# Performance work log

Hardware: AMD Instinct MI355X
Metric: run time of the kernel (lower is better)

The kernel has to match this reference:

```python
import jax, jax.numpy as jnp
import numpy as np

NF, NH1, NH21, NH22, NCLS = 6, 128, 128, 128, 3
OBS_X, OBS_Y, OBS_Z, R = 10.0, 10.0, 9.0, 7.0
BATCH = 131072


def setup_inputs() -> dict:
    key = jax.random.key(0)
    ks = jax.random.split(key, 16)
    def lin(kw, kb, fan_in, fan_out):
        bound = 1.0 / np.sqrt(fan_in)
        w = jax.random.uniform(kw, (fan_out, fan_in), jnp.float32, -bound, bound)
        b = jax.random.uniform(kb, (fan_out,), jnp.float32, -bound, bound)
        return w, b
    fc1_w, fc1_b = lin(ks[0], ks[1], NF, NH1)
    fc21_w, fc21_b = lin(ks[2], ks[3], NH1, NH21)
    fc22_w, fc22_b = lin(ks[4], ks[5], NH1, NH22)
    fcm1_w, fcm1_b = lin(ks[6], ks[7], NH21, NH21)
    fcm2_w, fcm2_b = lin(ks[8], ks[9], NH22, NH22)
    fc31_w, fc31_b = lin(ks[10], ks[11], NH21, NCLS)
    fc32_w, fc32_b = lin(ks[12], ks[13], NH22, 2)
    x = jax.random.normal(ks[14], (BATCH, NF), jnp.float32)
    mean = jnp.array([10.0, 0.0, 10.0, 0.0, 9.0, 0.0], jnp.float32)
    std = jnp.array([5.0, 2.0, 5.0, 2.0, 5.0, 2.0], jnp.float32)
    return {"x": x, "mean": mean, "std": std,
            "fc1_w": fc1_w, "fc1_b": fc1_b,
            "fc21_w": fc21_w, "fc21_b": fc21_b,
            "fc22_w": fc22_w, "fc22_b": fc22_b,
            "fcm1_w": fcm1_w, "fcm1_b": fcm1_b,
            "fcm2_w": fcm2_w, "fcm2_b": fcm2_b,
            "fc31_w": fc31_w, "fc31_b": fc31_b,
            "fc32_w": fc32_w, "fc32_b": fc32_b,
            "sgn": 1}


def _forward(x, mean, std, fc1_w, fc1_b, fc21_w, fc21_b, fc22_w, fc22_b,
             fcm1_w, fcm1_b, fcm2_w, fcm2_b, fc31_w, fc31_b, fc32_w, fc32_b):
    x0 = x * std + mean                                   # de-normalized state [B,6]
    h = jnp.tanh(x @ fc1_w.T + fc1_b)                     # [B,NH1]
    x21 = jnp.tanh(h @ fc21_w.T + fc21_b)
    x22 = jnp.tanh(h @ fc22_w.T + fc22_b)
    x21 = jnp.tanh(x21 @ fcm1_w.T + fcm1_b)
    x22 = jnp.tanh(x22 @ fcm2_w.T + fcm2_b)
    x31 = x21 @ fc31_w.T + fc31_b                         # QP linear term p, [B,3]
    x32 = 4.0 * jax.nn.sigmoid(x22 @ fc32_w.T + fc32_b)   # HOCBF penalties, [B,2]

    # higher-order CBF terms
    px, vx, py, vy, pz, vz = (x0[:, i] for i in range(6))
    dx, dy, dz = px - OBS_X, py - OBS_Y, pz - OBS_Z
    barrier = dx**4 + dy**4 + dz**4 - R**4
    barrier_dot = 4.0 * (dx**3 * vx + dy**3 * vy + dz**3 * vz)
    Lf2b = 12.0 * (dx**2 * vx**2 + dy**2 * vy**2 + dz**2 * vz**2)
    G = -4.0 * jnp.stack([dx**3, dy**3, dz**3], axis=-1)  # [B,3], single constraint G u <= h
    hvec = Lf2b + (x32[:, 0] + x32[:, 1]) * barrier_dot + x32[:, 0] * x32[:, 1] * barrier  # [B]

    # QP: min 0.5 u^T u + x31^T u  s.t.  G u <= h  (Q = I, one constraint)
    # Closed-form KKT: u = -x31 - lam*G, lam = max(0, (G @ (-x31) - h) / (G @ G))
    u_unc = -x31
    Gu = jnp.sum(G * u_unc, axis=-1)                      # [B]
    GG = jnp.sum(G * G, axis=-1)                          # [B]
    lam = jnp.maximum(Gu - hvec, 0.0) / GG
    u = u_unc - lam[:, None] * G                          # [B,3]
    return u


def reference(x, mean, std, fc1_w, fc1_b, fc21_w, fc21_b, fc22_w, fc22_b,
              fcm1_w, fcm1_b, fcm2_w, fcm2_b, fc31_w, fc31_b, fc32_w, fc32_b, sgn):
    return _forward(x, mean, std, fc1_w, fc1_b, fc21_w, fc21_b, fc22_w, fc22_b,
                    fcm1_w, fcm1_b, fcm2_w, fcm2_b, fc31_w, fc31_b, fc32_w, fc32_b)
```

## Files before the change

kernel.cpp:

```cpp
#include <hip/hip_runtime.h>

typedef _Float16 half8 __attribute__((ext_vector_type(8)));
typedef _Float16 half4_t __attribute__((ext_vector_type(4)));
typedef float float4_t __attribute__((ext_vector_type(4)));
typedef float float2_t __attribute__((ext_vector_type(2)));

#define SB 32
#define NT 256
#define RS (SB * 8)

#define OFF_W1   0
#define OFF_W21  4096
#define OFF_W22  20480
#define OFF_WM1  36864
#define OFF_WM2  53248
#define OFF_W4A  69632
#define OFF_BIAS 73728
#define WS_HELEMS 73728

__device__ __forceinline__ float fast_tanh(float x) {
  float e = __builtin_amdgcn_exp2f(x * 2.8853900817779268f);
  return fmaf(-2.f, __builtin_amdgcn_rcpf(1.f + e), 1.f);
}
__device__ __forceinline__ float sigmoid4(float z) {
  float e = __builtin_amdgcn_exp2f(-z * 1.4426950408889634f);
  return 4.f * __builtin_amdgcn_rcpf(1.f + e);
}

__global__ void prepack(const float* __restrict__ w1, const float* __restrict__ w21,
                        const float* __restrict__ w22, const float* __restrict__ wm1,
                        const float* __restrict__ wm2, const float* __restrict__ w31,
                        const float* __restrict__ w32, const float* __restrict__ b1,
                        const float* __restrict__ b21, const float* __restrict__ b22,
                        const float* __restrict__ bm1, const float* __restrict__ bm2,
                        _Float16* __restrict__ ws) {
  const int stride = gridDim.x * blockDim.x;
  for (int i = blockIdx.x * blockDim.x + threadIdx.x; i < WS_HELEMS; i += stride) {
    float v;
    if (i < OFF_W21) {
      int t = i;
      int j = t & 7, c = t >> 3, l16 = c & 15, t1 = c >> 4;
      int k8 = t1 & 3, mt = t1 >> 2;
      int row = mt * 16 + l16, k = k8 * 8 + j;
      v = (k < 6) ? w1[row * 6 + k] : 0.f;
    } else if (i < OFF_W4A) {
      int t = i - OFF_W21;
      int m = t >> 14; t &= 16383;
      const float* src = (m == 0) ? w21 : (m == 1) ? w22 : (m == 2) ? wm1 : wm2;
      int j = t & 7, c = t >> 3, l16 = c & 15, t1 = c >> 4;
      int k8 = t1 & 15, mt = t1 >> 4;
      v = src[(mt * 16 + l16) * 128 + k8 * 8 + j];
    } else {
      int t = i - OFF_W4A;
      int j = t & 7, r = t >> 3, l16 = r & 15, q = r >> 4;
      int cc = q & 15, chain = q >> 4;
      int k = cc * 8 + j, m = l16;
      if (chain == 0) v = (m < 3) ? w31[m * 128 + k] : 0.f;
      else            v = (m < 2) ? w32[m * 128 + k] : 0.f;
    }
    ws[i] = (_Float16)v;
  }
  float* bws = (float*)(ws + OFF_BIAS);
  for (int i = blockIdx.x * blockDim.x + threadIdx.x; i < 640; i += stride) {
    int layer = i >> 7, idx = i & 127;
    const float* src = (layer == 0) ? b1 : (layer == 1) ? b21
                     : (layer == 2) ? b22 : (layer == 3) ? bm1 : bm2;
    bws[i] = src[idx];
  }
}

__device__ __forceinline__ void gemm128(const _Float16* __restrict__ Wg,
                                        const float* __restrict__ biasG,
                                        const _Float16* __restrict__ inB,
                                        _Float16* __restrict__ outB,
                                        int quad, int l16, int mt0, int mt1) {
  const float4_t bv0 = *(const float4_t*)(biasG + mt0 * 16 + quad * 4);
  const float4_t bv1 = *(const float4_t*)(biasG + mt1 * 16 + quad * 4);
  half8 a0[4], a1[4];
#pragma unroll
  for (int kk = 0; kk < 4; ++kk) {
    a0[kk] = *(const half8*)(Wg + ((mt0 * 16 + kk * 4 + quad) * 16 + l16) * 8);
    a1[kk] = *(const half8*)(Wg + ((mt1 * 16 + kk * 4 + quad) * 16 + l16) * 8);
  }
  float4_t acc0[2], acc1[2];
#pragma unroll
  for (int nt = 0; nt < 2; ++nt) {
    acc0[nt] = (float4_t){0.f, 0.f, 0.f, 0.f};
    acc1[nt] = (float4_t){0.f, 0.f, 0.f, 0.f};
  }
#pragma unroll
  for (int kk = 0; kk < 4; ++kk) {
#pragma unroll
    for (int nt = 0; nt < 2; ++nt) {
      half8 b = *(const half8*)(inB + (kk * 4 + quad) * RS + (nt * 16 + l16) * 8);
      acc0[nt] = __builtin_amdgcn_mfma_f32_16x16x32_f16(a0[kk], b, acc0[nt], 0, 0, 0);
      acc1[nt] = __builtin_amdgcn_mfma_f32_16x16x32_f16(a1[kk], b, acc1[nt], 0, 0, 0);
    }
  }
  const int ob0 = mt0 * 16 + quad * 4;
  const int ob1 = mt1 * 16 + quad * 4;
#pragma unroll
  for (int nt = 0; nt < 2; ++nt) {
    const int s = nt * 16 + l16;
    half4_t h0, h1;
#pragma unroll
    for (int r = 0; r < 4; ++r) {
      h0[r] = (_Float16)fast_tanh(acc0[nt][r] + bv0[r]);
      h1[r] = (_Float16)fast_tanh(acc1[nt][r] + bv1[r]);
    }
    *(half4_t*)(outB + (ob0 >> 3) * RS + s * 8 + (ob0 & 7)) = h0;
    *(half4_t*)(outB + (ob1 >> 3) * RS + s * 8 + (ob1 & 7)) = h1;
  }
}

__global__ __launch_bounds__(NT, 6) void bnet_main(
    const float* __restrict__ x, const float* __restrict__ meang,
    const float* __restrict__ stdg, const float* __restrict__ b31,
    const float* __restrict__ b32, const _Float16* __restrict__ ws,
    float* __restrict__ out) {
  __shared__ __align__(16) _Float16 bufH[SB * 128];
  __shared__ __align__(16) _Float16 bufA[SB * 128];
  __shared__ __align__(16) _Float16 bufB[SB * 128];

  const int tid = threadIdx.x;
  const int wv = tid >> 6;
  const int lane = tid & 63;
  const int quad = lane >> 4;
  const int l16 = lane & 15;
  const int mt0 = wv * 2, mt1 = mt0 + 1;
  const int s0 = blockIdx.x * SB;
  const float* biasF = (const float*)(ws + OFF_BIAS);

  {
    half8 bx[2];
#pragma unroll
    for (int nt = 0; nt < 2; ++nt) {
      half8 v;
#pragma unroll
      for (int j = 0; j < 8; ++j) v[j] = (_Float16)0.f;
      if (quad == 0) {
        const float* xp = x + (size_t)(s0 + nt * 16 + l16) * 6;
        float2_t e0 = *(const float2_t*)(xp);
        float2_t e1 = *(const float2_t*)(xp + 2);
        float2_t e2 = *(const float2_t*)(xp + 4);
        v[0] = (_Float16)e0[0]; v[1] = (_Float16)e0[1];
        v[2] = (_Float16)e1[0]; v[3] = (_Float16)e1[1];
        v[4] = (_Float16)e2[0]; v[5] = (_Float16)e2[1];
      }
      bx[nt] = v;
    }
    const float4_t bv0 = *(const float4_t*)(biasF + mt0 * 16 + quad * 4);
    const float4_t bv1 = *(const float4_t*)(biasF + mt1 * 16 + quad * 4);
    half8 a0 = *(const half8*)(ws + OFF_W1 + ((mt0 * 4 + quad) * 16 + l16) * 8);
    half8 a1 = *(const half8*)(ws + OFF_W1 + ((mt1 * 4 + quad) * 16 + l16) * 8);
    float4_t acc0[2], acc1[2];
#pragma unroll
    for (int nt = 0; nt < 2; ++nt) {
      acc0[nt] = (float4_t){0.f, 0.f, 0.f, 0.f};
      acc1[nt] = (float4_t){0.f, 0.f, 0.f, 0.f};
      acc0[nt] = __builtin_amdgcn_mfma_f32_16x16x32_f16(a0, bx[nt], acc0[nt], 0, 0, 0);
      acc1[nt] = __builtin_amdgcn_mfma_f32_16x16x32_f16(a1, bx[nt], acc1[nt], 0, 0, 0);
    }
    const int ob0 = mt0 * 16 + quad * 4;
    const int ob1 = mt1 * 16 + quad * 4;
#pragma unroll
    for (int nt = 0; nt < 2; ++nt) {
      const int s = nt * 16 + l16;
      half4_t h0, h1;
#pragma unroll
      for (int r = 0; r < 4; ++r) {
        h0[r] = (_Float16)fast_tanh(acc0[nt][r] + bv0[r]);
        h1[r] = (_Float16)fast_tanh(acc1[nt][r] + bv1[r]);
      }
      *(half4_t*)(bufH + (ob0 >> 3) * RS + s * 8 + (ob0 & 7)) = h0;
      *(half4_t*)(bufH + (ob1 >> 3) * RS + s * 8 + (ob1 & 7)) = h1;
    }
  }
  __syncthreads();

  gemm128(ws + OFF_W21, biasF + 128, bufH, bufA, quad, l16, mt0, mt1);
  gemm128(ws + OFF_W22, biasF + 256, bufH, bufB, quad, l16, mt0, mt1);
  __syncthreads();
  gemm128(ws + OFF_WM1, biasF + 384, bufA, bufH, quad, l16, mt0, mt1);
  __syncthreads();
  gemm128(ws + OFF_WM2, biasF + 512, bufB, bufA, quad, l16, mt0, mt1);
  __syncthreads();

  if (wv == 0) {
    half8 a4[2][4];
#pragma unroll
    for (int c = 0; c < 2; ++c)
#pragma unroll
      for (int kk = 0; kk < 4; ++kk)
        a4[c][kk] = *(const half8*)(ws + OFF_W4A +
                                    ((c * 16 + kk * 4 + quad) * 16 + l16) * 8);
    float4_t acc[2][2];
#pragma unroll
    for (int c = 0; c < 2; ++c)
#pragma unroll
      for (int nt = 0; nt < 2; ++nt) acc[c][nt] = (float4_t){0.f, 0.f, 0.f, 0.f};
#pragma unroll
    for (int kk = 0; kk < 4; ++kk)
#pragma unroll
      for (int nt = 0; nt < 2; ++nt) {
        half8 b1f = *(const half8*)(bufH + (kk * 4 + quad) * RS + (nt * 16 + l16) * 8);
        half8 b2f = *(const half8*)(bufA + (kk * 4 + quad) * RS + (nt * 16 + l16) * 8);
        acc[0][nt] = __builtin_amdgcn_mfma_f32_16x16x32_f16(a4[0][kk], b1f, acc[0][nt], 0, 0, 0);
        acc[1][nt] = __builtin_amdgcn_mfma_f32_16x16x32_f16(a4[1][kk], b2f, acc[1][nt], 0, 0, 0);
      }
    if (quad == 0) {
      const float m0 = meang[0], m1 = meang[1], m2 = meang[2];
      const float m3 = meang[3], m4 = meang[4], m5 = meang[5];
      const float sd0 = stdg[0], sd1 = stdg[1], sd2 = stdg[2];
      const float sd3 = stdg[3], sd4 = stdg[4], sd5 = stdg[5];
      const float c31_0 = b31[0], c31_1 = b31[1], c31_2 = b31[2];
      const float c32_0 = b32[0], c32_1 = b32[1];
#pragma unroll
      for (int nt = 0; nt < 2; ++nt) {
        const int s = nt * 16 + l16;
        float u0 = -(acc[0][nt][0] + c31_0);
        float u1 = -(acc[0][nt][1] + c31_1);
        float u2 = -(acc[0][nt][2] + c31_2);
        float p0 = sigmoid4(acc[1][nt][0] + c32_0);
        float p1 = sigmoid4(acc[1][nt][1] + c32_1);
        const float* xp = x + (size_t)(s0 + s) * 6;
        float2_t e0 = *(const float2_t*)(xp);
        float2_t e1 = *(const float2_t*)(xp + 2);
        float2_t e2 = *(const float2_t*)(xp + 4);
        float px = e0[0] * sd0 + m0, vx = e0[1] * sd1 + m1;
        float py = e1[0] * sd2 + m2, vy = e1[1] * sd3 + m3;
        float pz = e2[0] * sd4 + m4, vz = e2[1] * sd5 + m5;
        float dx = px - 10.f, dy = py - 10.f, dz = pz - 9.f;
        float dx2 = dx * dx, dy2 = dy * dy, dz2 = dz * dz;
        float dx3 = dx2 * dx, dy3 = dy2 * dy, dz3 = dz2 * dz;
        float barrier = dx3 * dx + dy3 * dy + dz3 * dz - 2401.f;
        float bdot = 4.f * (dx3 * vx + dy3 * vy + dz3 * vz);
        float Lf2b = 12.f * (dx2 * vx * vx + dy2 * vy * vy + dz2 * vz * vz);
        float g0 = -4.f * dx3, g1 = -4.f * dy3, g2 = -4.f * dz3;
        float hv = Lf2b + (p0 + p1) * bdot + p0 * p1 * barrier;
        float Gu = g0 * u0 + g1 * u1 + g2 * u2;
        float GG = g0 * g0 + g1 * g1 + g2 * g2;
        float lam = fmaxf(Gu - hv, 0.f) / GG;
        float* op = out + (size_t)(s0 + s) * 3;
        op[0] = u0 - lam * g0;
        op[1] = u1 - lam * g1;
        op[2] = u2 - lam * g2;
      }
    }
  }
}

extern "C" void kernel_launch(void* const* d_in, const int* in_sizes, int n_in,
                              void* d_out, int out_size, void* d_ws, size_t ws_size,
                              hipStream_t stream) {
  const float* x    = (const float*)d_in[0];
  const float* mean = (const float*)d_in[1];
  const float* stdv = (const float*)d_in[2];
  const float* w1   = (const float*)d_in[3];
  const float* b1   = (const float*)d_in[4];
  const float* w21  = (const float*)d_in[5];
  const float* b21  = (const float*)d_in[6];
  const float* w22  = (const float*)d_in[7];
  const float* b22  = (const float*)d_in[8];
  const float* wm1  = (const float*)d_in[9];
  const float* bm1  = (const float*)d_in[10];
  const float* wm2  = (const float*)d_in[11];
  const float* bm2  = (const float*)d_in[12];
  const float* w31  = (const float*)d_in[13];
  const float* b31  = (const float*)d_in[14];
  const float* w32  = (const float*)d_in[15];
  const float* b32  = (const float*)d_in[16];
  _Float16* ws = (_Float16*)d_ws;
  float* out = (float*)d_out;
  const int batch = in_sizes[0] / 6;

  hipLaunchKernelGGL(prepack, dim3(96), dim3(NT), 0, stream,
                     w1, w21, w22, wm1, wm2, w31, w32,
                     b1, b21, b22, bm1, bm2, ws);
  hipLaunchKernelGGL(bnet_main, dim3(batch / SB), dim3(NT), 0, stream,
                     x, mean, stdv, b31, b32, (const _Float16*)ws, out);
}
```

Measured before the change: 133.4 us.

## Use 8 waves per block, fold tanh scaling into weights, prefetch weights

The block grows from 4 to 8 waves, so each wave computes a single 16-row M tile per layer, which halves per-wave MFMA and register work. The exp2 pre-scale constants for tanh and sigmoid are folded into the packed weights and biases, and biases now initialize the accumulators. A-fragments of later layers are loaded ahead of the barriers to overlap global loads with compute, and a fourth shared buffer removes one barrier. fp16 packing uses cvt_pkrtz (round toward zero). Launch bounds of (NT,6) with 512 threads may force heavy register limits or spills.

Result: faster. 126.4 us (-5.2%).

```diff
diff --git a/kernel.cpp b/kernel.cpp
--- a/kernel.cpp
+++ b/kernel.cpp
@@ -2,11 +2,12 @@
 
 typedef _Float16 half8 __attribute__((ext_vector_type(8)));
 typedef _Float16 half4_t __attribute__((ext_vector_type(4)));
+typedef __fp16 fp16x2 __attribute__((ext_vector_type(2)));
 typedef float float4_t __attribute__((ext_vector_type(4)));
 typedef float float2_t __attribute__((ext_vector_type(2)));
 
 #define SB 32
-#define NT 256
+#define NT 512
 #define RS (SB * 8)
 
 #define OFF_W1   0
@@ -18,13 +19,20 @@
 #define OFF_BIAS 73728
 #define WS_HELEMS 73728
 
-__device__ __forceinline__ float fast_tanh(float x) {
-  float e = __builtin_amdgcn_exp2f(x * 2.8853900817779268f);
+#define SCL_TANH 2.8853900817779268f
+#define SCL_SIG  -1.4426950408889634f
+
+__device__ __forceinline__ float tanh_pre(float a) {
+  float e = __builtin_amdgcn_exp2f(a);
   return fmaf(-2.f, __builtin_amdgcn_rcpf(1.f + e), 1.f);
 }
-__device__ __forceinline__ float sigmoid4(float z) {
-  float e = __builtin_amdgcn_exp2f(-z * 1.4426950408889634f);
-  return 4.f * __builtin_amdgcn_rcpf(1.f + e);
+__device__ __forceinline__ half4_t pack4(float v0, float v1, float v2, float v3) {
+  fp16x2 lo = __builtin_amdgcn_cvt_pkrtz(v0, v1);
+  fp16x2 hi = __builtin_amdgcn_cvt_pkrtz(v2, v3);
+  half4_t h;
+  h[0] = (_Float16)lo[0]; h[1] = (_Float16)lo[1];
+  h[2] = (_Float16)hi[0]; h[3] = (_Float16)hi[1];
+  return h;
 }
 
 __global__ void prepack(const float* __restrict__ w1, const float* __restrict__ w21,
@@ -42,21 +50,21 @@
       int j = t & 7, c = t >> 3, l16 = c & 15, t1 = c >> 4;
       int k8 = t1 & 3, mt = t1 >> 2;
       int row = mt * 16 + l16, k = k8 * 8 + j;
-      v = (k < 6) ? w1[row * 6 + k] : 0.f;
+      v = (k < 6) ? w1[row * 6 + k] * SCL_TANH : 0.f;
     } else if (i < OFF_W4A) {
       int t = i - OFF_W21;
       int m = t >> 14; t &= 16383;
       const float* src = (m == 0) ? w21 : (m == 1) ? w22 : (m == 2) ? wm1 : wm2;
       int j = t & 7, c = t >> 3, l16 = c & 15, t1 = c >> 4;
       int k8 = t1 & 15, mt = t1 >> 4;
-      v = src[(mt * 16 + l16) * 128 + k8 * 8 + j];
+      v = src[(mt * 16 + l16) * 128 + k8 * 8 + j] * SCL_TANH;
     } else {
       int t = i - OFF_W4A;
       int j = t & 7, r = t >> 3, l16 = r & 15, q = r >> 4;
       int cc = q & 15, chain = q >> 4;
       int k = cc * 8 + j, m = l16;
       if (chain == 0) v = (m < 3) ? w31[m * 128 + k] : 0.f;
-      else            v = (m < 2) ? w32[m * 128 + k] : 0.f;
+      else            v = (m < 2) ? w32[m * 128 + k] * SCL_SIG : 0.f;
     }
     ws[i] = (_Float16)v;
   }
@@ -65,51 +73,32 @@
     int layer = i >> 7, idx = i & 127;
     const float* src = (layer == 0) ? b1 : (layer == 1) ? b21
                      : (layer == 2) ? b22 : (layer == 3) ? bm1 : bm2;
-    bws[i] = src[idx];
-  }
-}
-
-__device__ __forceinline__ void gemm128(const _Float16* __restrict__ Wg,
-                                        const float* __restrict__ biasG,
-                                        const _Float16* __restrict__ inB,
-                                        _Float16* __restrict__ outB,
-                                        int quad, int l16, int mt0, int mt1) {
-  const float4_t bv0 = *(const float4_t*)(biasG + mt0 * 16 + quad * 4);
-  const float4_t bv1 = *(const float4_t*)(biasG + mt1 * 16 + quad * 4);
-  half8 a0[4], a1[4];
+    bws[i] = src[idx] * SCL_TANH;
+  }
+}
+
+__device__ __forceinline__ void layer128(const half8* __restrict__ A, float4_t bv,
+                                         const _Float16* __restrict__ inB,
+                                         _Float16* __restrict__ outB,
+                                         int quad, int l16, int wv) {
+  float4_t acc[2];
+  acc[0] = bv; acc[1] = bv;
 #pragma unroll
   for (int kk = 0; kk < 4; ++kk) {
-    a0[kk] = *(const half8*)(Wg + ((mt0 * 16 + kk * 4 + quad) * 16 + l16) * 8);
-    a1[kk] = *(const half8*)(Wg + ((mt1 * 16 + kk * 4 + quad) * 16 + l16) * 8);
-  }
-  float4_t acc0[2], acc1[2];
-#pragma unroll
-  for (int nt = 0; nt < 2; ++nt) {
-    acc0[nt] = (float4_t){0.f, 0.f, 0.f, 0.f};
-    acc1[nt] = (float4_t){0.f, 0.f, 0.f, 0.f};
-  }
-#pragma unroll
-  for (int kk = 0; kk < 4; ++kk) {
 #pragma unroll
     for (int nt = 0; nt < 2; ++nt) {
       half8 b = *(const half8*)(inB + (kk * 4 + quad) * RS + (nt * 16 + l16) * 8);
-      acc0[nt] = __builtin_amdgcn_mfma_f32_16x16x32_f16(a0[kk], b, acc0[nt], 0, 0, 0);
-      acc1[nt] = __builtin_amdgcn_mfma_f32_16x16x32_f16(a1[kk], b, acc1[nt], 0, 0, 0);
-    }
-  }
-  const int ob0 = mt0 * 16 + quad * 4;
-  const int ob1 = mt1 * 16 + quad * 4;
+      acc[nt] = __builtin_amdgcn_mfma_f32_16x16x32_f16(A[kk], b, acc[nt], 0, 0, 0);
+    }
+  }
+  const int ob = wv * 16 + quad * 4;
+  _Float16* base = outB + (ob >> 3) * RS + (ob & 7);
 #pragma unroll
   for (int nt = 0; nt < 2; ++nt) {
     const int s = nt * 16 + l16;
-    half4_t h0, h1;
-#pragma unroll
-    for (int r = 0; r < 4; ++r) {
-      h0[r] = (_Float16)fast_tanh(acc0[nt][r] + bv0[r]);
-      h1[r] = (_Float16)fast_tanh(acc1[nt][r] + bv1[r]);
-    }
-    *(half4_t*)(outB + (ob0 >> 3) * RS + s * 8 + (ob0 & 7)) = h0;
-    *(half4_t*)(outB + (ob1 >> 3) * RS + s * 8 + (ob1 & 7)) = h1;
+    half4_t h = pack4(tanh_pre(acc[nt][0]), tanh_pre(acc[nt][1]),
+                      tanh_pre(acc[nt][2]), tanh_pre(acc[nt][3]));
+    *(half4_t*)(base + s * 8) = h;
   }
 }
 
@@ -121,18 +110,31 @@
   __shared__ __align__(16) _Float16 bufH[SB * 128];
   __shared__ __align__(16) _Float16 bufA[SB * 128];
   __shared__ __align__(16) _Float16 bufB[SB * 128];
+  __shared__ __align__(16) _Float16 bufC[SB * 128];
 
   const int tid = threadIdx.x;
   const int wv = tid >> 6;
   const int lane = tid & 63;
   const int quad = lane >> 4;
   const int l16 = lane & 15;
-  const int mt0 = wv * 2, mt1 = mt0 + 1;
   const int s0 = blockIdx.x * SB;
   const float* biasF = (const float*)(ws + OFF_BIAS);
+  const int arow = (wv * 16 + quad * 4);
+
+  half8 A1 = *(const half8*)(ws + OFF_W1 + ((wv * 4 + quad) * 16 + l16) * 8);
+  float4_t bv1 = *(const float4_t*)(biasF + arow);
+  float4_t bv21 = *(const float4_t*)(biasF + 128 + arow);
+  float4_t bv22 = *(const float4_t*)(biasF + 256 + arow);
+  float4_t bvm1 = *(const float4_t*)(biasF + 384 + arow);
+  float4_t bvm2 = *(const float4_t*)(biasF + 512 + arow);
+  half8 A21[4];
+#pragma unroll
+  for (int kk = 0; kk < 4; ++kk)
+    A21[kk] = *(const half8*)(ws + OFF_W21 + ((wv * 16 + kk * 4 + quad) * 16 + l16) * 8);
 
   {
-    half8 bx[2];
+    float4_t acc[2];
+    acc[0] = bv1; acc[1] = bv1;
 #pragma unroll
     for (int nt = 0; nt < 2; ++nt) {
       half8 v;
@@ -147,82 +149,79 @@
         v[2] = (_Float16)e1[0]; v[3] = (_Float16)e1[1];
         v[4] = (_Float16)e2[0]; v[5] = (_Float16)e2[1];
       }
-      bx[nt] = v;
-    }
-    const float4_t bv0 = *(const float4_t*)(biasF + mt0 * 16 + quad * 4);
-    const float4_t bv1 = *(const float4_t*)(biasF + mt1 * 16 + quad * 4);
-    half8 a0 = *(const half8*)(ws + OFF_W1 + ((mt0 * 4 + quad) * 16 + l16) * 8);
-    half8 a1 = *(const half8*)(ws + OFF_W1 + ((mt1 * 4 + quad) * 16 + l16) * 8);
-    float4_t acc0[2], acc1[2];
-#pragma unroll
-    for (int nt = 0; nt < 2; ++nt) {
-      acc0[nt] = (float4_t){0.f, 0.f, 0.f, 0.f};
-      acc1[nt] = (float4_t){0.f, 0.f, 0.f, 0.f};
-      acc0[nt] = __builtin_amdgcn_mfma_f32_16x16x32_f16(a0, bx[nt], acc0[nt], 0, 0, 0);
-      acc1[nt] = __builtin_amdgcn_mfma_f32_16x16x32_f16(a1, bx[nt], acc1[nt], 0, 0, 0);
-    }
-    const int ob0 = mt0 * 16 + quad * 4;
-    const int ob1 = mt1 * 16 + quad * 4;
+      acc[nt] = __builtin_amdgcn_mfma_f32_16x16x32_f16(A1, v, acc[nt], 0, 0, 0);
+    }
+    _Float16* base = bufH + (arow >> 3) * RS + (arow & 7);
 #pragma unroll
     for (int nt = 0; nt < 2; ++nt) {
       const int s = nt * 16 + l16;
-      half4_t h0, h1;
-#pragma unroll
-      for (int r = 0; r < 4; ++r) {
-        h0[r] = (_Float16)fast_tanh(acc0[nt][r] + bv0[r]);
-        h1[r] = (_Float16)fast_tanh(acc1[nt][r] + bv1[r]);
-      }
-      *(half4_t*)(bufH + (ob0 >> 3) * RS + s * 8 + (ob0 & 7)) = h0;
-      *(half4_t*)(bufH + (ob1 >> 3) * RS + s * 8 + (ob1 & 7)) = h1;
-    }
-  }
+      half4_t h = pack4(tanh_pre(acc[nt][0]), tanh_pre(acc[nt][1]),
+                        tanh_pre(acc[nt][2]), tanh_pre(acc[nt][3]));
+      *(half4_t*)(base + s * 8) = h;
+    }
+  }
+  half8 A22[4];
+#pragma unroll
+  for (int kk = 0; kk < 4; ++kk)
+    A22[kk] = *(const half8*)(ws + OFF_W22 + ((wv * 16 + kk * 4 + quad) * 16 + l16) * 8);
   __syncthreads();
 
-  gemm128(ws + OFF_W21, biasF + 128, bufH, bufA, quad, l16, mt0, mt1);
-  gemm128(ws + OFF_W22, biasF + 256, bufH, bufB, quad, l16, mt0, mt1);
+  layer128(A21, bv21, bufH, bufA, quad, l16, wv);
+  half8 AM1[4];
+#pragma unroll
+  for (int kk = 0; kk < 4; ++kk)
+    AM1[kk] = *(const half8*)(ws + OFF_WM1 + ((wv * 16 + kk * 4 + quad) * 16 + l16) * 8);
+  layer128(A22, bv22, bufH, bufB, quad, l16, wv);
   __syncthreads();
-  gemm128(ws + OFF_WM1, biasF + 384, bufA, bufH, quad, l16, mt0, mt1);
+
+  half8 AM2[4];
+#pragma unroll
+  for (int kk = 0; kk < 4; ++kk)
+    AM2[kk] = *(const half8*)(ws + OFF_WM2 + ((wv * 16 + kk * 4 + quad) * 16 + l16) * 8);
+  layer128(AM1, bvm1, bufA, bufH, quad, l16, wv);
+  layer128(AM2, bvm2, bufB, bufC, quad, l16, wv);
   __syncthreads();
-  gemm128(ws + OFF_WM2, biasF + 512, bufB, bufA, quad, l16, mt0, mt1);
-  __syncthreads();
 
   if (wv == 0) {
-    half8 a4[2][4];
+    half8 A4[2][4];
 #pragma unroll
     for (int c = 0; c < 2; ++c)
 #pragma unroll
       for (int kk = 0; kk < 4; ++kk)
-        a4[c][kk] = *(const half8*)(ws + OFF_W4A +
+        A4[c][kk] = *(const half8*)(ws + OFF_W4A +
                                     ((c * 16 + kk * 4 + quad) * 16 + l16) * 8);
-    float4_t acc[2][2];
-#pragma unroll
-    for (int c = 0; c < 2; ++c)
-#pragma unroll
-      for (int nt = 0; nt < 2; ++nt) acc[c][nt] = (float4_t){0.f, 0.f, 0.f, 0.f};
+    float4_t a0[2], a1[2];
+#pragma unroll
+    for (int nt = 0; nt < 2; ++nt) {
+      a0[nt] = (float4_t){0.f, 0.f, 0.f, 0.f};
+      a1[nt] = (float4_t){0.f, 0.f, 0.f, 0.f};
+      if (quad == 0) {
+        a0[nt][0] = b31[0]; a0[nt][1] = b31[1]; a0[nt][2] = b31[2];
+        a1[nt][0] = b32[0] * SCL_SIG; a1[nt][1] = b32[1] * SCL_SIG;
+      }
+    }
 #pragma unroll
     for (int kk = 0; kk < 4; ++kk)
 #pragma unroll
       for (int nt = 0; nt < 2; ++nt) {
-        half8 b1f = *(const half8*)(bufH + (kk * 4 + quad) * RS + (nt * 16 + l16) * 8);
-        half8 b2f = *(const half8*)(bufA + (kk * 4 + quad) * RS + (nt * 16 + l16) * 8);
-        acc[0][nt] = __builtin_amdgcn_mfma_f32_16x16x32_f16(a4[0][kk], b1f, acc[0][nt], 0, 0, 0);
-        acc[1][nt] = __builtin_amdgcn_mfma_f32_16x16x32_f16(a4[1][kk], b2f, acc[1][nt], 0, 0, 0);
+        half8 bh = *(const half8*)(bufH + (kk * 4 + quad) * RS + (nt * 16 + l16) * 8);
+        half8 bc = *(const half8*)(bufC + (kk * 4 + quad) * RS + (nt * 16 + l16) * 8);
+        a0[nt] = __builtin_amdgcn_mfma_f32_16x16x32_f16(A4[0][kk], bh, a0[nt], 0, 0, 0);
+        a1[nt] = __builtin_amdgcn_mfma_f32_16x16x32_f16(A4[1][kk], bc, a1[nt], 0, 0, 0);
       }
     if (quad == 0) {
       const float m0 = meang[0], m1 = meang[1], m2 = meang[2];
       const float m3 = meang[3], m4 = meang[4], m5 = meang[5];
       const float sd0 = stdg[0], sd1 = stdg[1], sd2 = stdg[2];
       const float sd3 = stdg[3], sd4 = stdg[4], sd5 = stdg[5];
-      const float c31_0 = b31[0], c31_1 = b31[1], c31_2 = b31[2];
-      const float c32_0 = b32[0], c32_1 = b32[1];
 #pragma unroll
       for (int nt = 0; nt < 2; ++nt) {
         const int s = nt * 16 + l16;
-        float u0 = -(acc[0][nt][0] + c31_0);
-        float u1 = -(acc[0][nt][1] + c31_1);
-        float u2 = -(acc[0][nt][2] + c31_2);
-        float p0 = sigmoid4(acc[1][nt][0] + c32_0);
-        float p1 = sigmoid4(acc[1][nt][1] + c32_1);
+        float u0 = -a0[nt][0];
+        float u1 = -a0[nt][1];
+        float u2 = -a0[nt][2];
+        float p0 = 4.f * __builtin_amdgcn_rcpf(1.f + __builtin_amdgcn_exp2f(a1[nt][0]));
+        float p1 = 4.f * __builtin_amdgcn_rcpf(1.f + __builtin_amdgcn_exp2f(a1[nt][1]));
         const float* xp = x + (size_t)(s0 + s) * 6;
         float2_t e0 = *(const float2_t*)(xp);
         float2_t e1 = *(const float2_t*)(xp + 2);
@@ -274,7 +273,7 @@
   float* out = (float*)d_out;
   const int batch = in_sizes[0] / 6;
 
-  hipLaunchKernelGGL(prepack, dim3(96), dim3(NT), 0, stream,
+  hipLaunchKernelGGL(prepack, dim3(96), dim3(256), 0, stream,
                      w1, w21, w22, wm1, wm2, w31, w32,
                      b1, b21, b22, bm1, bm2, ws);
   hipLaunchKernelGGL(bnet_main, dim3(batch / SB), dim3(NT), 0, stream,
```
